# Kernel optimization log

Hardware: AMD Instinct MI355X
Metric: run time of the kernel (lower is better)

## Reference

```python
import jax, jax.numpy as jnp
import numpy as np

B, V, D, H, ET = 64, 64, 64, 64, 2  # batch, num_vars, input_dim, hidden, edge_types


def setup_inputs() -> dict:
    key = jax.random.key(0)
    ks = jax.random.split(key, 6)
    adj = np.ones((V, V)) - np.eye(V)
    send, recv = np.where(adj)  # E = V*(V-1) = 4032 edges, row-major order as in torch code
    E = send.shape[0]
    s = 0.05
    return {
        "inputs": jax.random.normal(ks[0], (B, V, D), jnp.float32),
        "edges": jax.random.uniform(ks[1], (B, E, ET), jnp.float32),
        "W1": jax.random.normal(ks[2], (ET, H, 2 * D), jnp.float32) * s,
        "b1": jnp.zeros((ET, H), jnp.float32),
        "W2": jax.random.normal(ks[3], (ET, H, H), jnp.float32) * s,
        "b2": jnp.zeros((ET, H), jnp.float32),
        "send_idx": jnp.asarray(send, jnp.int32),
        "recv_idx": jnp.asarray(recv, jnp.int32),
    }


def reference(inputs, edges, W1, b1, W2, b2, send_idx, recv_idx):
    # gather node features onto edges: [B, E, 2D]
    pre_msg = jnp.concatenate([inputs[:, recv_idx, :], inputs[:, send_idx, :]], axis=-1)
    all_msgs = jnp.zeros((pre_msg.shape[0], pre_msg.shape[1], H), pre_msg.dtype)
    # skip_first_edge_type=True -> start at 1; eval mode -> dropout p=0 (identity)
    for i in range(1, ET):
        msg = jax.nn.relu(jnp.einsum('bef,hf->beh', pre_msg, W1[i]) + b1[i])
        msg = jax.nn.relu(jnp.einsum('beh,oh->beo', msg, W2[i]) + b2[i])
        all_msgs = all_msgs + msg * edges[:, :, i:i + 1]
    # onehot-matmul aggregation == scatter-sum of edge messages into receiver nodes
    agg_msgs = jnp.zeros((inputs.shape[0], V, H), all_msgs.dtype).at[:, recv_idx, :].add(all_msgs)
    return jnp.concatenate([inputs, agg_msgs], axis=-1)  # [B, V, D+H]
```

## Files before the change

### kernel.cpp

```cpp
#include <hip/hip_runtime.h>
#include <hip/hip_bf16.h>

#define NB 64
#define NV 64
#define ND 64
#define NH 64
#define NE 4032
#define OUTW 128

typedef __bf16 bf16_t;
typedef bf16_t bf16x8 __attribute__((ext_vector_type(8)));
typedef float f32x4 __attribute__((ext_vector_type(4)));

__global__ void prep2(const float* __restrict__ inputs,
                      const float* __restrict__ W1,
                      const float* __restrict__ b1,
                      const float* __restrict__ W2,
                      float* __restrict__ Yb,
                      bf16_t* __restrict__ Zb,
                      bf16_t* __restrict__ wf2) {
    const int blk = blockIdx.x;
    const int tid = threadIdx.x;
    if (blk == NB) {
        #pragma unroll
        for (int q = 0; q < 16; ++q) {
            int u = tid * 16 + q;
            int j = u & 7, lane = (u >> 3) & 63, ks = (u >> 9) & 1, nt = (u >> 10) & 3;
            int n = 16 * nt + (lane & 15);
            int h = 32 * ks + 8 * (lane >> 4) + j;
            wf2[u] = (bf16_t)W2[(NH + n) * NH + h];
        }
        return;
    }
    const int b = blk;
    const int lane = tid & 63, wid = tid >> 6, lr = lane & 15, lg = lane >> 4;

    const float* xrow = inputs + (b * NV + 16 * wid + lr) * ND;
    bf16x8 a[2];
    #pragma unroll
    for (int ks = 0; ks < 2; ++ks) {
        f32x4 v0 = *(const f32x4*)(xrow + 32 * ks + 8 * lg);
        f32x4 v1 = *(const f32x4*)(xrow + 32 * ks + 8 * lg + 4);
        bf16x8 t;
        #pragma unroll
        for (int q = 0; q < 4; ++q) { t[q] = (bf16_t)v0[q]; t[4 + q] = (bf16_t)v1[q]; }
        a[ks] = t;
    }

    f32x4 accY[4], accZ[4];
    #pragma unroll
    for (int nt = 0; nt < 4; ++nt) {
        float base = b1[NH + 16 * nt + lr];
        accY[nt] = (f32x4){base, base, base, base};
        accZ[nt] = (f32x4){0.f, 0.f, 0.f, 0.f};
    }
    #pragma unroll
    for (int nt = 0; nt < 4; ++nt) {
        const float* wrow = W1 + (NH + 16 * nt + lr) * (2 * ND);
        #pragma unroll
        for (int ks = 0; ks < 2; ++ks) {
            f32x4 u0 = *(const f32x4*)(wrow + 32 * ks + 8 * lg);
            f32x4 u1 = *(const f32x4*)(wrow + 32 * ks + 8 * lg + 4);
            f32x4 w0 = *(const f32x4*)(wrow + 64 + 32 * ks + 8 * lg);
            f32x4 w1 = *(const f32x4*)(wrow + 64 + 32 * ks + 8 * lg + 4);
            bf16x8 by, bz;
            #pragma unroll
            for (int q = 0; q < 4; ++q) {
                by[q] = (bf16_t)u0[q]; by[4 + q] = (bf16_t)u1[q];
                bz[q] = (bf16_t)w0[q]; bz[4 + q] = (bf16_t)w1[q];
            }
            accY[nt] = __builtin_amdgcn_mfma_f32_16x16x32_bf16(a[ks], by, accY[nt], 0, 0, 0);
            accZ[nt] = __builtin_amdgcn_mfma_f32_16x16x32_bf16(a[ks], bz, accZ[nt], 0, 0, 0);
        }
    }
    #pragma unroll
    for (int nt = 0; nt < 4; ++nt) {
        #pragma unroll
        for (int j = 0; j < 4; ++j) {
            int v = 16 * wid + 4 * lg + j;
            Yb[(b * NV + v) * NH + 16 * nt + lr] = accY[nt][j];
            Zb[(b * NV + v) * NH + 16 * nt + lr] = (bf16_t)accZ[nt][j];
        }
    }
}

__global__ __launch_bounds__(64, 4)
void gnn_main2(const float* __restrict__ inputs,
               const float* __restrict__ edges,
               const float* __restrict__ b2,
               const float* __restrict__ Yb,
               const bf16_t* __restrict__ Zb,
               const bf16_t* __restrict__ wf2,
               float* __restrict__ out) {
    const int bid = blockIdx.x;
    const int b = bid >> 6, r = bid & 63;
    const int lane = threadIdx.x;
    const int lr = lane & 15, lg = lane >> 4;

    bf16x8 wb[4][2];
    #pragma unroll
    for (int nt = 0; nt < 4; ++nt)
        #pragma unroll
        for (int ks = 0; ks < 2; ++ks)
            wb[nt][ks] = *(const bf16x8*)(wf2 + ((nt * 2 + ks) * 64 + lane) * 8);

    const float* ybr = Yb + (b * NV + r) * NH;
    f32x4 y[2][2];
    #pragma unroll
    for (int ks = 0; ks < 2; ++ks) {
        y[ks][0] = *(const f32x4*)(ybr + 32 * ks + 8 * lg);
        y[ks][1] = *(const f32x4*)(ybr + 32 * ks + 8 * lg + 4);
    }

    float base[4];
    #pragma unroll
    for (int nt = 0; nt < 4; ++nt) base[nt] = b2[NH + 16 * nt + lr];

    const bf16_t* zb = Zb + b * NV * NH;
    const float* eb = edges + b * NE * 2;

    float psum[4] = {0.f, 0.f, 0.f, 0.f};

    #pragma unroll
    for (int mt = 0; mt < 4; ++mt) {
        const int m = 16 * mt + lr;
        const int s = (m < r) ? m : (m == 63 ? r : m + 1);

        bf16x8 afr[2];
        #pragma unroll
        for (int ks = 0; ks < 2; ++ks) {
            bf16x8 z = *(const bf16x8*)(zb + s * NH + 32 * ks + 8 * lg);
            bf16x8 t;
            #pragma unroll
            for (int q = 0; q < 8; ++q) {
                float vv = (float)z[q] + y[ks][q >> 2][q & 3];
                t[q] = (bf16_t)(vv > 0.f ? vv : 0.f);
            }
            afr[ks] = t;
        }

        float wj[4];
        #pragma unroll
        for (int j = 0; j < 4; ++j) {
            int me = 16 * mt + 4 * lg + j;
            float w = 0.f;
            if (me < 63) {
                int se = (me < r) ? me : me + 1;
                int e = se * 63 + r - (se < r ? 1 : 0);
                w = eb[e * 2 + 1];
            }
            wj[j] = w;
        }

        #pragma unroll
        for (int nt = 0; nt < 4; ++nt) {
            f32x4 acc = (f32x4){base[nt], base[nt], base[nt], base[nt]};
            acc = __builtin_amdgcn_mfma_f32_16x16x32_bf16(afr[0], wb[nt][0], acc, 0, 0, 0);
            acc = __builtin_amdgcn_mfma_f32_16x16x32_bf16(afr[1], wb[nt][1], acc, 0, 0, 0);
            float ss = 0.f;
            #pragma unroll
            for (int j = 0; j < 4; ++j) {
                float v = acc[j];
                v = v > 0.f ? v : 0.f;
                ss = fmaf(v, wj[j], ss);
            }
            psum[nt] += ss;
        }
    }

    #pragma unroll
    for (int nt = 0; nt < 4; ++nt) {
        psum[nt] += __shfl_xor(psum[nt], 16);
        psum[nt] += __shfl_xor(psum[nt], 32);
    }

    float* o = out + (b * NV + r) * OUTW;
    o[lane] = inputs[(b * NV + r) * ND + lane];
    float v = (lg == 0) ? psum[0] : (lg == 1) ? psum[1] : (lg == 2) ? psum[2] : psum[3];
    o[ND + lane] = v;
}

extern "C" void kernel_launch(void* const* d_in, const int* in_sizes, int n_in,
                              void* d_out, int out_size, void* d_ws, size_t ws_size,
                              hipStream_t stream) {
    const float* inputs = (const float*)d_in[0];
    const float* edges  = (const float*)d_in[1];
    const float* W1     = (const float*)d_in[2];
    const float* b1     = (const float*)d_in[3];
    const float* W2     = (const float*)d_in[4];
    const float* b2     = (const float*)d_in[5];

    float*  Yb  = (float*)d_ws;
    bf16_t* Zb  = (bf16_t*)(Yb + NB * NV * NH);
    bf16_t* wf2 = Zb + NB * NV * NH;
    float*  out = (float*)d_out;

    prep2<<<NB + 1, 256, 0, stream>>>(inputs, W1, b1, W2, Yb, Zb, wf2);
    gnn_main2<<<NB * NV, 64, 0, stream>>>(inputs, edges, b2, Yb, Zb, wf2, out);
}
```

Baseline: 23.89 us.

## Fuse layer-1 precompute into main GNN kernel using LDS staging

Merges the precompute kernel and the per-receiver message kernel into one launch. Each block recomputes the first-layer node projections for its batch into shared memory and stages the edge weights there, then processes 8 receivers across 4 wavefronts. This removes the second launch and the global workspace round trip, at the cost of computing layer-1 eight times per batch and loading W2 in every block.

```diff
diff --git a/kernel.cpp b/kernel.cpp
--- a/kernel.cpp
+++ b/kernel.cpp
@@ -12,172 +12,169 @@
 typedef bf16_t bf16x8 __attribute__((ext_vector_type(8)));
 typedef float f32x4 __attribute__((ext_vector_type(4)));
 
-__global__ void prep2(const float* __restrict__ inputs,
-                      const float* __restrict__ W1,
-                      const float* __restrict__ b1,
-                      const float* __restrict__ W2,
-                      float* __restrict__ Yb,
-                      bf16_t* __restrict__ Zb,
-                      bf16_t* __restrict__ wf2) {
+__global__ __launch_bounds__(256, 2)
+void gnn_fused(const float* __restrict__ inputs,
+               const float* __restrict__ edges,
+               const float* __restrict__ W1,
+               const float* __restrict__ b1,
+               const float* __restrict__ W2,
+               const float* __restrict__ b2,
+               float* __restrict__ out) {
+    __shared__ float  Ylds[NV][NH + 1];
+    __shared__ bf16_t Zlds[NV][NH + 8];
+    __shared__ float  EW[NE];
+
     const int blk = blockIdx.x;
+    const int b = blk >> 3, oct = blk & 7;
     const int tid = threadIdx.x;
-    if (blk == NB) {
-        #pragma unroll
-        for (int q = 0; q < 16; ++q) {
-            int u = tid * 16 + q;
-            int j = u & 7, lane = (u >> 3) & 63, ks = (u >> 9) & 1, nt = (u >> 10) & 3;
-            int n = 16 * nt + (lane & 15);
-            int h = 32 * ks + 8 * (lane >> 4) + j;
-            wf2[u] = (bf16_t)W2[(NH + n) * NH + h];
-        }
-        return;
-    }
-    const int b = blk;
-    const int lane = tid & 63, wid = tid >> 6, lr = lane & 15, lg = lane >> 4;
+    const int lane = tid & 63, wid = tid >> 6;
+    const int lr = lane & 15, lg = lane >> 4;
 
-    const float* xrow = inputs + (b * NV + 16 * wid + lr) * ND;
-    bf16x8 a[2];
+    const float2* e2 = (const float2*)(edges + b * NE * 2);
     #pragma unroll
-    for (int ks = 0; ks < 2; ++ks) {
-        f32x4 v0 = *(const f32x4*)(xrow + 32 * ks + 8 * lg);
-        f32x4 v1 = *(const f32x4*)(xrow + 32 * ks + 8 * lg + 4);
-        bf16x8 t;
-        #pragma unroll
-        for (int q = 0; q < 4; ++q) { t[q] = (bf16_t)v0[q]; t[4 + q] = (bf16_t)v1[q]; }
-        a[ks] = t;
+    for (int i = 0; i < 16; ++i) {
+        int e = i * 256 + tid;
+        if (e < NE) EW[e] = e2[e].y;
     }
 
-    f32x4 accY[4], accZ[4];
+    bf16x8 wb[4][2];
+    float base2[4];
     #pragma unroll
     for (int nt = 0; nt < 4; ++nt) {
-        float base = b1[NH + 16 * nt + lr];
-        accY[nt] = (f32x4){base, base, base, base};
-        accZ[nt] = (f32x4){0.f, 0.f, 0.f, 0.f};
-    }
-    #pragma unroll
-    for (int nt = 0; nt < 4; ++nt) {
-        const float* wrow = W1 + (NH + 16 * nt + lr) * (2 * ND);
+        base2[nt] = b2[NH + 16 * nt + lr];
+        const float* w2row = W2 + (NH + 16 * nt + lr) * NH;
         #pragma unroll
         for (int ks = 0; ks < 2; ++ks) {
-            f32x4 u0 = *(const f32x4*)(wrow + 32 * ks + 8 * lg);
-            f32x4 u1 = *(const f32x4*)(wrow + 32 * ks + 8 * lg + 4);
-            f32x4 w0 = *(const f32x4*)(wrow + 64 + 32 * ks + 8 * lg);
-            f32x4 w1 = *(const f32x4*)(wrow + 64 + 32 * ks + 8 * lg + 4);
-            bf16x8 by, bz;
+            f32x4 v0 = *(const f32x4*)(w2row + 32 * ks + 8 * lg);
+            f32x4 v1 = *(const f32x4*)(w2row + 32 * ks + 8 * lg + 4);
+            bf16x8 t;
             #pragma unroll
-            for (int q = 0; q < 4; ++q) {
-                by[q] = (bf16_t)u0[q]; by[4 + q] = (bf16_t)u1[q];
-                bz[q] = (bf16_t)w0[q]; bz[4 + q] = (bf16_t)w1[q];
-            }
-            accY[nt] = __builtin_amdgcn_mfma_f32_16x16x32_bf16(a[ks], by, accY[nt], 0, 0, 0);
-            accZ[nt] = __builtin_amdgcn_mfma_f32_16x16x32_bf16(a[ks], bz, accZ[nt], 0, 0, 0);
+            for (int q = 0; q < 4; ++q) { t[q] = (bf16_t)v0[q]; t[4 + q] = (bf16_t)v1[q]; }
+            wb[nt][ks] = t;
         }
     }
-    #pragma unroll
-    for (int nt = 0; nt < 4; ++nt) {
+
+    {
+        const float* xrow = inputs + (b * NV + 16 * wid + lr) * ND;
+        bf16x8 a[2];
         #pragma unroll
-        for (int j = 0; j < 4; ++j) {
-            int v = 16 * wid + 4 * lg + j;
-            Yb[(b * NV + v) * NH + 16 * nt + lr] = accY[nt][j];
-            Zb[(b * NV + v) * NH + 16 * nt + lr] = (bf16_t)accZ[nt][j];
+        for (int ks = 0; ks < 2; ++ks) {
+            f32x4 v0 = *(const f32x4*)(xrow + 32 * ks + 8 * lg);
+            f32x4 v1 = *(const f32x4*)(xrow + 32 * ks + 8 * lg + 4);
+            bf16x8 t;
+            #pragma unroll
+            for (int q = 0; q < 4; ++q) { t[q] = (bf16_t)v0[q]; t[4 + q] = (bf16_t)v1[q]; }
+            a[ks] = t;
+        }
+
+        f32x4 accY[4], accZ[4];
+        #pragma unroll
+        for (int nt = 0; nt < 4; ++nt) {
+            float base = b1[NH + 16 * nt + lr];
+            accY[nt] = (f32x4){base, base, base, base};
+            accZ[nt] = (f32x4){0.f, 0.f, 0.f, 0.f};
+        }
+        #pragma unroll
+        for (int nt = 0; nt < 4; ++nt) {
+            const float* wrow = W1 + (NH + 16 * nt + lr) * (2 * ND);
+            #pragma unroll
+            for (int ks = 0; ks < 2; ++ks) {
+                f32x4 u0 = *(const f32x4*)(wrow + 32 * ks + 8 * lg);
+                f32x4 u1 = *(const f32x4*)(wrow + 32 * ks + 8 * lg + 4);
+                f32x4 w0 = *(const f32x4*)(wrow + 64 + 32 * ks + 8 * lg);
+                f32x4 w1 = *(const f32x4*)(wrow + 64 + 32 * ks + 8 * lg + 4);
+                bf16x8 by, bz;
+                #pragma unroll
+                for (int q = 0; q < 4; ++q) {
+                    by[q] = (bf16_t)u0[q]; by[4 + q] = (bf16_t)u1[q];
+                    bz[q] = (bf16_t)w0[q]; bz[4 + q] = (bf16_t)w1[q];
+                }
+                accY[nt] = __builtin_amdgcn_mfma_f32_16x16x32_bf16(a[ks], by, accY[nt], 0, 0, 0);
+                accZ[nt] = __builtin_amdgcn_mfma_f32_16x16x32_bf16(a[ks], bz, accZ[nt], 0, 0, 0);
+            }
+        }
+        #pragma unroll
+        for (int nt = 0; nt < 4; ++nt) {
+            #pragma unroll
+            for (int j = 0; j < 4; ++j) {
+                int v = 16 * wid + 4 * lg + j;
+                Ylds[v][16 * nt + lr] = accY[nt][j];
+                Zlds[v][16 * nt + lr] = (bf16_t)accZ[nt][j];
+            }
         }
     }
-}
-
-__global__ __launch_bounds__(64, 4)
-void gnn_main2(const float* __restrict__ inputs,
-               const float* __restrict__ edges,
-               const float* __restrict__ b2,
-               const float* __restrict__ Yb,
-               const bf16_t* __restrict__ Zb,
-               const bf16_t* __restrict__ wf2,
-               float* __restrict__ out) {
-    const int bid = blockIdx.x;
-    const int b = bid >> 6, r = bid & 63;
-    const int lane = threadIdx.x;
-    const int lr = lane & 15, lg = lane >> 4;
-
-    bf16x8 wb[4][2];
-    #pragma unroll
-    for (int nt = 0; nt < 4; ++nt)
-        #pragma unroll
-        for (int ks = 0; ks < 2; ++ks)
-            wb[nt][ks] = *(const bf16x8*)(wf2 + ((nt * 2 + ks) * 64 + lane) * 8);
-
-    const float* ybr = Yb + (b * NV + r) * NH;
-    f32x4 y[2][2];
-    #pragma unroll
-    for (int ks = 0; ks < 2; ++ks) {
-        y[ks][0] = *(const f32x4*)(ybr + 32 * ks + 8 * lg);
-        y[ks][1] = *(const f32x4*)(ybr + 32 * ks + 8 * lg + 4);
-    }
-
-    float base[4];
-    #pragma unroll
-    for (int nt = 0; nt < 4; ++nt) base[nt] = b2[NH + 16 * nt + lr];
-
-    const bf16_t* zb = Zb + b * NV * NH;
-    const float* eb = edges + b * NE * 2;
-
-    float psum[4] = {0.f, 0.f, 0.f, 0.f};
+    __syncthreads();
 
     #pragma unroll
-    for (int mt = 0; mt < 4; ++mt) {
-        const int m = 16 * mt + lr;
-        const int s = (m < r) ? m : (m == 63 ? r : m + 1);
+    for (int rr = 0; rr < 2; ++rr) {
+        const int r = oct * 8 + wid * 2 + rr;
 
-        bf16x8 afr[2];
+        f32x4 y[2][2];
         #pragma unroll
         for (int ks = 0; ks < 2; ++ks) {
-            bf16x8 z = *(const bf16x8*)(zb + s * NH + 32 * ks + 8 * lg);
-            bf16x8 t;
-            #pragma unroll
-            for (int q = 0; q < 8; ++q) {
-                float vv = (float)z[q] + y[ks][q >> 2][q & 3];
-                t[q] = (bf16_t)(vv > 0.f ? vv : 0.f);
-            }
-            afr[ks] = t;
+            y[ks][0] = *(const f32x4*)(&Ylds[r][32 * ks + 8 * lg]);
+            y[ks][1] = *(const f32x4*)(&Ylds[r][32 * ks + 8 * lg + 4]);
         }
 
-        float wj[4];
+        float psum[4] = {0.f, 0.f, 0.f, 0.f};
+
         #pragma unroll
-        for (int j = 0; j < 4; ++j) {
-            int me = 16 * mt + 4 * lg + j;
-            float w = 0.f;
-            if (me < 63) {
-                int se = (me < r) ? me : me + 1;
-                int e = se * 63 + r - (se < r ? 1 : 0);
-                w = eb[e * 2 + 1];
+        for (int mt = 0; mt < 4; ++mt) {
+            const int m = 16 * mt + lr;
+            const int s = (m < r) ? m : (m == 63 ? r : m + 1);
+
+            bf16x8 afr[2];
+            #pragma unroll
+            for (int ks = 0; ks < 2; ++ks) {
+                bf16x8 z = *(const bf16x8*)(&Zlds[s][32 * ks + 8 * lg]);
+                bf16x8 t;
+                #pragma unroll
+                for (int q = 0; q < 8; ++q) {
+                    float vv = (float)z[q] + y[ks][q >> 2][q & 3];
+                    t[q] = (bf16_t)(vv > 0.f ? vv : 0.f);
+                }
+                afr[ks] = t;
             }
-            wj[j] = w;
+
+            float wj[4];
+            #pragma unroll
+            for (int j = 0; j < 4; ++j) {
+                int me = 16 * mt + 4 * lg + j;
+                float w = 0.f;
+                if (me < 63) {
+                    int se = (me < r) ? me : me + 1;
+                    w = EW[se * 63 + r - (se < r ? 1 : 0)];
+                }
+                wj[j] = w;
+            }
+
+            #pragma unroll
+            for (int nt = 0; nt < 4; ++nt) {
+                f32x4 acc = (f32x4){base2[nt], base2[nt], base2[nt], base2[nt]};
+                acc = __builtin_amdgcn_mfma_f32_16x16x32_bf16(afr[0], wb[nt][0], acc, 0, 0, 0);
+                acc = __builtin_amdgcn_mfma_f32_16x16x32_bf16(afr[1], wb[nt][1], acc, 0, 0, 0);
+                float ss = 0.f;
+                #pragma unroll
+                for (int j = 0; j < 4; ++j) {
+                    float v = acc[j];
+                    v = v > 0.f ? v : 0.f;
+                    ss = fmaf(v, wj[j], ss);
+                }
+                psum[nt] += ss;
+            }
         }
 
         #pragma unroll
         for (int nt = 0; nt < 4; ++nt) {
-            f32x4 acc = (f32x4){base[nt], base[nt], base[nt], base[nt]};
-            acc = __builtin_amdgcn_mfma_f32_16x16x32_bf16(afr[0], wb[nt][0], acc, 0, 0, 0);
-            acc = __builtin_amdgcn_mfma_f32_16x16x32_bf16(afr[1], wb[nt][1], acc, 0, 0, 0);
-            float ss = 0.f;
-            #pragma unroll
-            for (int j = 0; j < 4; ++j) {
-                float v = acc[j];
-                v = v > 0.f ? v : 0.f;
-                ss = fmaf(v, wj[j], ss);
-            }
-            psum[nt] += ss;
+            psum[nt] += __shfl_xor(psum[nt], 16);
+            psum[nt] += __shfl_xor(psum[nt], 32);
         }
+
+        float* o = out + (b * NV + r) * OUTW;
+        o[lane] = inputs[(b * NV + r) * ND + lane];
+        float v = (lg == 0) ? psum[0] : (lg == 1) ? psum[1] : (lg == 2) ? psum[2] : psum[3];
+        o[ND + lane] = v;
     }
-
-    #pragma unroll
-    for (int nt = 0; nt < 4; ++nt) {
-        psum[nt] += __shfl_xor(psum[nt], 16);
-        psum[nt] += __shfl_xor(psum[nt], 32);
-    }
-
-    float* o = out + (b * NV + r) * OUTW;
-    o[lane] = inputs[(b * NV + r) * ND + lane];
-    float v = (lg == 0) ? psum[0] : (lg == 1) ? psum[1] : (lg == 2) ? psum[2] : psum[3];
-    o[ND + lane] = v;
 }
 
 extern "C" void kernel_launch(void* const* d_in, const int* in_sizes, int n_in,
@@ -190,11 +187,5 @@
     const float* W2     = (const float*)d_in[4];
     const float* b2     = (const float*)d_in[5];
 
-    float*  Yb  = (float*)d_ws;
-    bf16_t* Zb  = (bf16_t*)(Yb + NB * NV * NH);
-    bf16_t* wf2 = Zb + NB * NV * NH;
-    float*  out = (float*)d_out;
-
-    prep2<<<NB + 1, 256, 0, stream>>>(inputs, W1, b1, W2, Yb, Zb, wf2);
-    gnn_main2<<<NB * NV, 64, 0, stream>>>(inputs, edges, b2, Yb, Zb, wf2, out);
+    gnn_fused<<<NB * 8, 256, 0, stream>>>(inputs, edges, W1, b1, W2, b2, (float*)d_out);
 }
```

After: 22.48 us. -5.9%, faster.
